# Kernel optimization log

Hardware: AMD Instinct MI355X
Metric: run time of the kernel (lower is better)

## Reference

```python
import jax, jax.numpy as jnp
import numpy as np

DK, DV, NH, KS, STRIDE = 256, 256, 8, 3, 1
PAD = (KS - 1) // 2


def conv1d(x, w, b, stride=1, pad=PAD):
    # x: (B, Cin, W), w: (Cout, Cin, K)
    y = jax.lax.conv_general_dilated(
        x, w, window_strides=(stride,), padding=[(pad, pad)],
        dimension_numbers=("NCH", "OIH", "NCH"))
    return y + b[None, :, None]


def setup_inputs() -> dict:
    key = jax.random.key(0)
    ks = jax.random.split(key, 7)
    B, C, W = 8, 256, 2048
    OUT = 512
    x = jax.random.normal(ks[0], (B, C, W), dtype=jnp.float32)
    w_conv = jax.random.normal(ks[1], (OUT - DV, C, KS), dtype=jnp.float32) * 0.05
    b_conv = jax.random.normal(ks[2], (OUT - DV,), dtype=jnp.float32) * 0.05
    w_qkv = jax.random.normal(ks[3], (2 * DK + DV, C, KS), dtype=jnp.float32) * 0.05
    b_qkv = jax.random.normal(ks[4], (2 * DK + DV,), dtype=jnp.float32) * 0.05
    w_attn = jax.random.normal(ks[5], (DV, DV), dtype=jnp.float32) * 0.05
    b_attn = jax.random.normal(ks[6], (DV,), dtype=jnp.float32) * 0.05
    return {"x": x, "w_conv": w_conv, "b_conv": b_conv,
            "w_qkv": w_qkv, "b_qkv": b_qkv,
            "w_attn": w_attn, "b_attn": b_attn}


def reference(x, w_conv, b_conv, w_qkv, b_qkv, w_attn, b_attn):
    B, _, _ = x.shape
    dkh, dvh = DK // NH, DV // NH

    conv_out = conv1d(x, w_conv, b_conv, stride=STRIDE)   # (B, out-dv, W)
    W_out = conv_out.shape[-1]

    qkv = conv1d(x, w_qkv, b_qkv, stride=STRIDE)          # (B, 2dk+dv, W)
    q, k, v = jnp.split(qkv, [DK, 2 * DK], axis=1)
    q = q.reshape(B, NH, dkh, W_out) * (dkh ** -0.5)      # flat_q
    k = k.reshape(B, NH, dkh, W_out)                      # flat_k
    v = v.reshape(B, NH, dvh, W_out)                      # flat_v

    # logits = flat_q^T @ flat_k : (B, NH, W, W)
    logits = jnp.einsum("bhdq,bhdk->bhqk", q, k)
    weights = jax.nn.softmax(logits, axis=-1)
    # attn = weights @ flat_v^T : (B, NH, W, dvh)
    attn = jnp.einsum("bhqk,bhdk->bhqd", weights, v)
    # NOTE: original torch code RESHAPES (B,NH,W,dvh)->(B,NH,dvh,1,W) (no transpose),
    # then combines heads to (B, NH*dvh, 1, W). Reproduce faithfully:
    attn = attn.reshape(B, DV, W_out)
    # 1x1 conv on attention output
    attn = jnp.einsum("oc,bcw->bow", w_attn, attn) + b_attn[None, :, None]

    return jnp.concatenate([conv_out, attn], axis=1)      # (B, out_channels, W)
```

## Files before the change

kernel.cpp:

```cpp
#include <hip/hip_runtime.h>

typedef _Float16 f16;
typedef _Float16 f16x8 __attribute__((ext_vector_type(8)));
typedef _Float16 f16x4 __attribute__((ext_vector_type(4)));
typedef _Float16 f16x2 __attribute__((ext_vector_type(2)));
typedef __fp16 fp16x2 __attribute__((ext_vector_type(2)));
typedef float f32x4 __attribute__((ext_vector_type(4)));

static __device__ __forceinline__ f32x4 mfma32(f16x8 a, f16x8 b, f32x4 c) {
  return __builtin_amdgcn_mfma_f32_16x16x32_f16(a, b, c, 0, 0, 0);
}
static __device__ __forceinline__ void gload16(const void* g, void* l) {
  __builtin_amdgcn_global_load_lds(
      (const __attribute__((address_space(1))) unsigned int*)g,
      (__attribute__((address_space(3))) unsigned int*)l, 16, 0, 0);
}
static __device__ __forceinline__ f16x2 exp2pk(float a, float b) {
  union { fp16x2 i; f16x2 o; } u;
  u.i = __builtin_amdgcn_cvt_pkrtz(__builtin_amdgcn_exp2f(a), __builtin_amdgcn_exp2f(b));
  return u.o;
}
static __device__ __forceinline__ f16x8 cat4(f16x2 a, f16x2 b, f16x2 c, f16x2 d) {
  union { f16x2 h2[4]; f16x8 h8; } u;
  u.h2[0] = a; u.h2[1] = b; u.h2[2] = c; u.h2[3] = d;
  return u.h8;
}

#define QSCALE_L2 0.25503626336707584f
#define SH_L2  12.98425536800067f

#define OFF_XT   0
#define OFF_WP   8396800
#define OFF_WA   9969664
#define OFF_BIAS 10100736
#define OFF_Q    10104832
#define OFF_K    18493440
#define OFF_V    26882048
#define OFF_AT   35270656

__global__ __launch_bounds__(256) void prep_x_kernel(const float* __restrict__ x,
                                                     f16* __restrict__ xTc) {
  if (blockIdx.x == 256) {
    for (int i = threadIdx.x; i < 4096; i += 256) {
      int b = i >> 9, r = (i >> 8) & 1, ck = (i >> 5) & 7, ci = i & 31;
      xTc[((size_t)(b * 8 + ck) * 2050 + (r ? 2049 : 0)) * 32 + ci] = (f16)0.f;
    }
    return;
  }
  __shared__ f16 tl[64][258];
  const int b  = blockIdx.x >> 5;
  const int w0 = (blockIdx.x & 31) * 64;
  const int tid = threadIdx.x;

  {
    const int wi = (tid & 15) * 4;
    const int cb = tid >> 4;
#pragma unroll 4
    for (int p = 0; p < 16; ++p) {
      const int c = cb + p * 16;
      const float4 v = *(const float4*)(x + ((size_t)(b * 256 + c) * 2048 + w0 + wi));
      tl[wi + 0][c] = (f16)v.x;
      tl[wi + 1][c] = (f16)v.y;
      tl[wi + 2][c] = (f16)v.z;
      tl[wi + 3][c] = (f16)v.w;
    }
  }
  __syncthreads();

  {
    const int w   = tid >> 2;
    const int ci8 = (tid & 3) * 8;
#pragma unroll
    for (int cgk = 0; cgk < 8; ++cgk) {
      f16x8 v = *(const f16x8*)(&tl[w][cgk * 32 + ci8]);
      *(f16x8*)(xTc + ((size_t)(b * 8 + cgk) * 2050 + 1 + w0 + w) * 32 + ci8) = v;
    }
  }
}

__global__ void prep_w_kernel(const float* __restrict__ wc, const float* __restrict__ bc,
                              const float* __restrict__ wq, const float* __restrict__ bq,
                              const float* __restrict__ wa_in,
                              f16* __restrict__ wpc, f16* __restrict__ wa,
                              float* __restrict__ biasp) {
  const int bid = blockIdx.x, tid = threadIdx.x;
  if (bid < 3072) {
    const int n = bid & 1023, t = bid >> 10, c = tid;
    float v;
    if (n < 256) {
      v = wc[(n * 256 + c) * 3 + t];
    } else {
      const int j = n - 256;
      v = wq[((size_t)j * 256 + c) * 3 + t];
      if (j < 256) v *= QSCALE_L2;
    }
    wpc[((size_t)(t * 8 + (c >> 5)) * 1024 + n) * 32 + (c & 31)] = (f16)v;
  } else if (bid < 3328) {
    const int o = bid - 3072;
    wa[o * 256 + tid] = (f16)wa_in[o * 256 + tid];
  } else {
    for (int n = tid; n < 1024; n += 256) {
      float v = (n < 256) ? bc[n] : ((n < 512) ? bq[n - 256] * QSCALE_L2 : bq[n - 256]);
      biasp[n] = v;
    }
  }
}

__global__ __launch_bounds__(512, 1) void conv_kernel(
    const f16* __restrict__ xTc, const f16* __restrict__ wpc,
    const float* __restrict__ biasp, float* __restrict__ out,
    f16* __restrict__ q_ws, f16* __restrict__ k_ws, f16* __restrict__ v_pk) {
  __shared__ __align__(16) char smA[65536];
  __shared__ __align__(16) char smB[65536];

  const int fid = blockIdx.x;
  const int b   = fid & 7;
  const int g   = fid >> 3;
  const int ocb = (g & 3) * 256;
  const int wb  = (g >> 2) * 256;
  const int tid = threadIdx.x;
  const int wid = tid >> 6, l = tid & 63, lr = l & 15, lg = l >> 4;
  const int wm = wid >> 2, wn = wid & 3;

  f32x4 acc[8][4];
#pragma unroll
  for (int i = 0; i < 8; ++i)
#pragma unroll
    for (int j = 0; j < 4; ++j) acc[i][j] = (f32x4){0.f, 0.f, 0.f, 0.f};

  const int swu = (tid >> 2) * 64 + (((tid & 3) ^ ((tid >> 3) & 3)) * 16);
  const char* agb = (const char*)xTc + (size_t)b * 1049600 + (size_t)wb * 64 + swu;
  const char* bgb = (const char*)wpc + (size_t)ocb * 64 + swu;

  const int sx   = ((lr >> 1) & 3) << 4;
  const int foa0 = (wm * 128 + lr) * 64 + ((lg * 16) ^ sx);
  const int fob0 = (wn * 64 + lr) * 64 + ((lg * 16) ^ sx);

  auto stageA = [&](int kt, int kk) {
    const int t = kt >> 2, ck = ((kt & 3) << 1) | kk;
    const char* src = agb + (size_t)ck * 131200 + t * 64;
    char* dst = smA + ((2 * kt + kk) & 3) * 16384 + tid * 16;
    gload16(src, dst);
    gload16(src + 8192, dst + 8192);
  };
  auto stageB = [&](int kt, int kk) {
    const int t = kt >> 2, ck = ((kt & 3) << 1) | kk;
    const char* src = bgb + (size_t)(t * 8 + ck) * 65536;
    char* dst = smB + ((2 * kt + kk) & 3) * 16384 + tid * 16;
    gload16(src, dst);
    gload16(src + 8192, dst + 8192);
  };

  auto phase = [&](int kt, int mh, int kk) {
    const int slot = (2 * kt + kk) & 3;
    const char* ab = smA + slot * 16384;
    const char* bb = smB + slot * 16384;
    f16x8 af[4], bf[4];
#pragma unroll
    for (int mt = 0; mt < 4; ++mt) af[mt] = *(const f16x8*)(ab + foa0 + mh * 4096 + mt * 1024);
#pragma unroll
    for (int nt = 0; nt < 4; ++nt) bf[nt] = *(const f16x8*)(bb + fob0 + nt * 1024);
    __builtin_amdgcn_s_setprio(1);
#pragma unroll
    for (int mt = 0; mt < 4; ++mt)
#pragma unroll
      for (int nt = 0; nt < 4; ++nt)
        acc[mh * 4 + mt][nt] = mfma32(af[mt], bf[nt], acc[mh * 4 + mt][nt]);
    __builtin_amdgcn_s_setprio(0);
  };

#define VMW(n) asm volatile("s_waitcnt vmcnt(" #n ")" ::: "memory")
#define BAR()  __builtin_amdgcn_s_barrier()
#define SCB()  __builtin_amdgcn_sched_barrier(0)

  stageA(0, 0); stageB(0, 0); stageA(0, 1); stageB(0, 1);

#pragma unroll 1
  for (int kt = 0; kt < 11; ++kt) {
    stageA(kt + 1, 0); VMW(6); BAR(); SCB(); phase(kt, 0, 0);
    stageB(kt + 1, 0);         BAR(); SCB(); phase(kt, 1, 0);
    stageA(kt + 1, 1); VMW(6); BAR(); SCB(); phase(kt, 0, 1);
    stageB(kt + 1, 1);         BAR(); SCB(); phase(kt, 1, 1);
  }
  VMW(4); BAR(); SCB(); phase(11, 0, 0);
          BAR(); SCB(); phase(11, 1, 0);
  VMW(0); BAR(); SCB(); phase(11, 0, 1);
          BAR(); SCB(); phase(11, 1, 1);

#undef VMW
#undef BAR
#undef SCB

#pragma unroll
  for (int nt = 0; nt < 4; ++nt) {
    const int oc = ocb + wn * 64 + nt * 16 + lr;
    const float bias = biasp[oc];
#pragma unroll
    for (int am = 0; am < 8; ++am) {
      const int w0 = wb + wm * 128 + am * 16 + lg * 4;
      const float v0 = acc[am][nt][0] + bias;
      const float v1 = acc[am][nt][1] + bias;
      const float v2 = acc[am][nt][2] + bias;
      const float v3 = acc[am][nt][3] + bias;
      if (oc < 256) {
        float4 o4 = {v0, v1, v2, v3};
        *(float4*)(out + (size_t)(b * 512 + oc) * 2048 + w0) = o4;
      } else if (oc < 768) {
        const int d  = oc - 256;
        f16* dst = (d < 256) ? q_ws : k_ws;
        const int dd = d & 31, h = (d >> 5) & 7;
        f16* p = dst + (size_t)((b * 8 + h) * 2048 + w0) * 32 + dd;
        p[0]  = (f16)v0;
        p[32] = (f16)v1;
        p[64] = (f16)v2;
        p[96] = (f16)v3;
      } else {
        const int d = oc - 768;
        const int dd = d & 31, h = d >> 5;
        f16x4 o4 = {(f16)v0, (f16)v1, (f16)v2, (f16)v3};
        *(f16x4*)(v_pk + (size_t)(b * 8 + h) * 65536 +
                  (w0 >> 7) * 4096 + ((w0 >> 5) & 3) * 1024 + dd * 32 +
                  ((w0 >> 2) & 3) * 8 + ((w0 & 16) ? 4 : 0)) = o4;
      }
    }
  }
}

__global__ __launch_bounds__(512, 4) void attn_kernel(
    const f16* __restrict__ q_ws, const f16* __restrict__ k_ws,
    const f16* __restrict__ v_pk, f16* __restrict__ aT) {
  __shared__ __align__(16) f16 Kl[2][4096];
  __shared__ __align__(16) f16 Vl[2][4096];

  const int fid = blockIdx.x;
  const int qb  = fid >> 6;
  const int bh  = ((fid & 7) << 3) | ((fid >> 3) & 7);
  const int tid = threadIdx.x, wid = tid >> 6, l = tid & 63, lr = l & 15, lg = l >> 4;
  const int b = bh >> 3, h = bh & 7;
  const size_t qk_base = (size_t)bh * 2048 * 32;

  const int u = tid & 255;
  const char* gp = (tid < 256)
      ? (const char*)(k_ws + qk_base) + (u >> 2) * 64 + ((u & 3) ^ ((u >> 3) & 3)) * 16
      : (const char*)(v_pk + (size_t)bh * 65536) + u * 16;
  char* lp = ((tid < 256) ? (char*)(&Kl[0][0]) : (char*)(&Vl[0][0])) + u * 16;

  const int qrow0 = qb * 256 + wid * 32;
  f16x8 qf0 = *(const f16x8*)(q_ws + qk_base + (size_t)(qrow0 + lr) * 32 + lg * 8);
  f16x8 qf1 = *(const f16x8*)(q_ws + qk_base + (size_t)(qrow0 + 16 + lr) * 32 + lg * 8);

  f32x4 accO[2][2];
  f32x4 ssum[2];
#pragma unroll
  for (int i = 0; i < 2; ++i) {
    ssum[i] = (f32x4){0.f, 0.f, 0.f, 0.f};
#pragma unroll
    for (int j = 0; j < 2; ++j) accO[i][j] = (f32x4){0.f, 0.f, 0.f, 0.f};
  }
  const f32x4 minit = {-SH_L2, -SH_L2, -SH_L2, -SH_L2};
  const f16x8 ones8 = {(f16)1.f, (f16)1.f, (f16)1.f, (f16)1.f,
                       (f16)1.f, (f16)1.f, (f16)1.f, (f16)1.f};

  const int kfo = lr * 64 + ((lg * 16) ^ (((lr >> 1) & 3) << 4));
  const int vfo = lr * 64 + lg * 16;

  auto stage = [&](int pb) {
    gload16(gp,        lp + pb * 8192);
    gload16(gp + 4096, lp + pb * 8192 + 4096);
    gp += 8192;
  };

  auto compute = [&](int pb) {
    const char* kbuf = (const char*)(&Kl[0][0]) + pb * 8192;
    const char* vbuf = (const char*)(&Vl[0][0]) + pb * 8192;
    f32x4 s0[8], s1[8];
    __builtin_amdgcn_s_setprio(1);
#pragma unroll
    for (int mt = 0; mt < 8; ++mt) {
      f16x8 kf = *(const f16x8*)(kbuf + kfo + mt * 1024);
      s0[mt] = mfma32(kf, qf0, minit);
      s1[mt] = mfma32(kf, qf1, minit);
    }
    __builtin_amdgcn_s_setprio(0);
#pragma unroll
    for (int ksq = 0; ksq < 4; ++ksq) {
      f16x8 pa0 = cat4(exp2pk(s0[2*ksq][0], s0[2*ksq][1]), exp2pk(s0[2*ksq][2], s0[2*ksq][3]),
                       exp2pk(s0[2*ksq+1][0], s0[2*ksq+1][1]), exp2pk(s0[2*ksq+1][2], s0[2*ksq+1][3]));
      f16x8 pa1 = cat4(exp2pk(s1[2*ksq][0], s1[2*ksq][1]), exp2pk(s1[2*ksq][2], s1[2*ksq][3]),
                       exp2pk(s1[2*ksq+1][0], s1[2*ksq+1][1]), exp2pk(s1[2*ksq+1][2], s1[2*ksq+1][3]));
      f16x8 vf0 = *(const f16x8*)(vbuf + vfo + ksq * 2048);
      f16x8 vf1 = *(const f16x8*)(vbuf + vfo + ksq * 2048 + 1024);
      __builtin_amdgcn_s_setprio(1);
      accO[0][0] = mfma32(vf0, pa0, accO[0][0]);
      accO[0][1] = mfma32(vf0, pa1, accO[0][1]);
      accO[1][0] = mfma32(vf1, pa0, accO[1][0]);
      accO[1][1] = mfma32(vf1, pa1, accO[1][1]);
      ssum[0] = mfma32(ones8, pa0, ssum[0]);
      ssum[1] = mfma32(ones8, pa1, ssum[1]);
      __builtin_amdgcn_s_setprio(0);
    }
  };

#define VMW(n) asm volatile("s_waitcnt vmcnt(" #n ")" ::: "memory")
#define BAR()  __builtin_amdgcn_s_barrier()
#define SCB()  __builtin_amdgcn_sched_barrier(0)

  stage(0);
#pragma unroll 1
  for (int t = 0; t < 15; ++t) {
    stage((t + 1) & 1);
    VMW(2); BAR(); SCB();
    compute(t & 1);
    BAR();
  }
  VMW(0); BAR(); SCB();
  compute(1);

#pragma unroll
  for (int nt = 0; nt < 2; ++nt) {
    const float inv = 1.f / ssum[nt][0];
    const int q = qrow0 + nt * 16 + lr;
    const int cc = h * 32 + (q >> 6);
    const int wr = (q & 63) * 32;
#pragma unroll
    for (int dvt = 0; dvt < 2; ++dvt)
#pragma unroll
      for (int r = 0; r < 4; ++r) {
        const int dv = dvt * 16 + lg * 4 + r;
        aT[((size_t)b * 2048 + wr + dv) * 256 + cc] = (f16)(accO[dvt][nt][r] * inv);
      }
  }
#undef VMW
#undef BAR
#undef SCB
}

__global__ __launch_bounds__(256, 4) void proj_kernel(
    const f16* __restrict__ aT, const f16* __restrict__ wa,
    const float* __restrict__ b_attn, float* __restrict__ out) {
  const int fid = blockIdx.x;
  const int b  = fid & 7;
  const int g  = fid >> 3;
  const int ob = (g & 1) * 128;
  const int wb = (g >> 1) * 128;
  const int tid = threadIdx.x;
  const int wid = tid >> 6, l = tid & 63, lr = l & 15, lg = l >> 4;
  const int wm = wid >> 1, wn = wid & 1;

  f32x4 acc[4][4];
#pragma unroll
  for (int i = 0; i < 4; ++i)
#pragma unroll
    for (int j = 0; j < 4; ++j) acc[i][j] = (f32x4){0.f, 0.f, 0.f, 0.f};

  const f16* ab = aT + (size_t)(b * 2048 + wb + wm * 64 + lr) * 256 + lg * 8;
  const f16* wb_p = wa + (size_t)(ob + wn * 64 + lr) * 256 + lg * 8;

  for (int ks = 0; ks < 8; ++ks) {
    const int co = ks * 32;
    f16x8 af[4], bf[4];
#pragma unroll
    for (int mt = 0; mt < 4; ++mt) af[mt] = *(const f16x8*)(ab + (size_t)mt * 16 * 256 + co);
#pragma unroll
    for (int nt = 0; nt < 4; ++nt) bf[nt] = *(const f16x8*)(wb_p + (size_t)nt * 16 * 256 + co);
    __builtin_amdgcn_s_setprio(1);
#pragma unroll
    for (int mt = 0; mt < 4; ++mt)
#pragma unroll
      for (int nt = 0; nt < 4; ++nt) acc[mt][nt] = mfma32(af[mt], bf[nt], acc[mt][nt]);
    __builtin_amdgcn_s_setprio(0);
  }

#pragma unroll
  for (int nt = 0; nt < 4; ++nt) {
    const int o = ob + wn * 64 + nt * 16 + lr;
    const float bias = b_attn[o];
#pragma unroll
    for (int mt = 0; mt < 4; ++mt) {
      const int w0 = wb + wm * 64 + mt * 16 + lg * 4;
      float4 o4 = {acc[mt][nt][0] + bias, acc[mt][nt][1] + bias,
                   acc[mt][nt][2] + bias, acc[mt][nt][3] + bias};
      *(float4*)(out + (size_t)(b * 512 + 256 + o) * 2048 + w0) = o4;
    }
  }
}

extern "C" void kernel_launch(void* const* d_in, const int* in_sizes, int n_in,
                              void* d_out, int out_size, void* d_ws, size_t ws_size,
                              hipStream_t stream) {
  const float* x      = (const float*)d_in[0];
  const float* w_conv = (const float*)d_in[1];
  const float* b_conv = (const float*)d_in[2];
  const float* w_qkv  = (const float*)d_in[3];
  const float* b_qkv  = (const float*)d_in[4];
  const float* w_attn = (const float*)d_in[5];
  const float* b_attn = (const float*)d_in[6];
  float* out = (float*)d_out;

  char* ws = (char*)d_ws;
  f16*   xTc   = (f16*)(ws + OFF_XT);
  f16*   wpc   = (f16*)(ws + OFF_WP);
  f16*   wa    = (f16*)(ws + OFF_WA);
  float* biasp = (float*)(ws + OFF_BIAS);
  f16*   q_ws  = (f16*)(ws + OFF_Q);
  f16*   k_ws  = (f16*)(ws + OFF_K);
  f16*   v_pk  = (f16*)(ws + OFF_V);
  f16*   aT    = (f16*)(ws + OFF_AT);

  prep_x_kernel<<<257, 256, 0, stream>>>(x, xTc);
  prep_w_kernel<<<3329, 256, 0, stream>>>(w_conv, b_conv, w_qkv, b_qkv, w_attn, wpc, wa, biasp);
  conv_kernel<<<256, 512, 0, stream>>>(xTc, wpc, biasp, out, q_ws, k_ws, v_pk);
  attn_kernel<<<512, 512, 0, stream>>>(q_ws, k_ws, v_pk, aT);
  proj_kernel<<<256, 256, 0, stream>>>(aT, wa, b_attn, out);
}
```

Baseline: 115.2 us.

## Split K and V tile staging to interleave loads with QK and PV phases

The attention loop now issues the K and V tile prefetches separately, with all 512 threads loading one 16-byte chunk of each instead of two half-block groups. The next K tile is issued before the QK^T MFMAs and the next V tile after them, with a wait and barrier before each phase in place of a barrier after the combined compute. The goal is finer-grained overlap of global-to-LDS traffic with the two MFMA phases and shorter stalls on each barrier. The trade-off is more waitcnt/barrier points inside the loop and score registers kept live across the phase split, which may add pressure or serialization.

Result: no change. 116.1 us (+0.7%).

```diff
diff --git a/kernel.cpp b/kernel.cpp
--- a/kernel.cpp
+++ b/kernel.cpp
@@ -239,11 +239,11 @@
   const int b = bh >> 3, h = bh & 7;
   const size_t qk_base = (size_t)bh * 2048 * 32;
 
-  const int u = tid & 255;
-  const char* gp = (tid < 256)
-      ? (const char*)(k_ws + qk_base) + (u >> 2) * 64 + ((u & 3) ^ ((u >> 3) & 3)) * 16
-      : (const char*)(v_pk + (size_t)bh * 65536) + u * 16;
-  char* lp = ((tid < 256) ? (char*)(&Kl[0][0]) : (char*)(&Vl[0][0])) + u * 16;
+  const char* kgp = (const char*)(k_ws + qk_base) +
+                    (tid >> 2) * 64 + ((tid & 3) ^ ((tid >> 3) & 3)) * 16;
+  const char* vgp = (const char*)(v_pk + (size_t)bh * 65536) + tid * 16;
+  char* klp = (char*)(&Kl[0][0]) + tid * 16;
+  char* vlp = (char*)(&Vl[0][0]) + tid * 16;
 
   const int qrow0 = qb * 256 + wid * 32;
   f16x8 qf0 = *(const f16x8*)(q_ws + qk_base + (size_t)(qrow0 + lr) * 32 + lg * 8);
@@ -264,16 +264,13 @@
   const int kfo = lr * 64 + ((lg * 16) ^ (((lr >> 1) & 3) << 4));
   const int vfo = lr * 64 + lg * 16;
 
-  auto stage = [&](int pb) {
-    gload16(gp,        lp + pb * 8192);
-    gload16(gp + 4096, lp + pb * 8192 + 4096);
-    gp += 8192;
-  };
-
-  auto compute = [&](int pb) {
+  auto stageK = [&](int pb) { gload16(kgp, klp + pb * 8192); kgp += 8192; };
+  auto stageV = [&](int pb) { gload16(vgp, vlp + pb * 8192); vgp += 8192; };
+
+  f32x4 s0[8], s1[8];
+
+  auto qk = [&](int pb) {
     const char* kbuf = (const char*)(&Kl[0][0]) + pb * 8192;
-    const char* vbuf = (const char*)(&Vl[0][0]) + pb * 8192;
-    f32x4 s0[8], s1[8];
     __builtin_amdgcn_s_setprio(1);
 #pragma unroll
     for (int mt = 0; mt < 8; ++mt) {
@@ -282,6 +279,10 @@
       s1[mt] = mfma32(kf, qf1, minit);
     }
     __builtin_amdgcn_s_setprio(0);
+  };
+
+  auto pv = [&](int pb) {
+    const char* vbuf = (const char*)(&Vl[0][0]) + pb * 8192;
 #pragma unroll
     for (int ksq = 0; ksq < 4; ++ksq) {
       f16x8 pa0 = cat4(exp2pk(s0[2*ksq][0], s0[2*ksq][1]), exp2pk(s0[2*ksq][2], s0[2*ksq][3]),
@@ -305,16 +306,20 @@
 #define BAR()  __builtin_amdgcn_s_barrier()
 #define SCB()  __builtin_amdgcn_sched_barrier(0)
 
-  stage(0);
+  stageK(0); stageV(0);
 #pragma unroll 1
   for (int t = 0; t < 15; ++t) {
-    stage((t + 1) & 1);
+    stageK((t + 1) & 1);
     VMW(2); BAR(); SCB();
-    compute(t & 1);
-    BAR();
-  }
+    qk(t & 1);
+    stageV((t + 1) & 1);
+    VMW(2); BAR(); SCB();
+    pv(t & 1);
+  }
+  VMW(1); BAR(); SCB();
+  qk(1);
   VMW(0); BAR(); SCB();
-  compute(1);
+  pv(1);
 
 #pragma unroll
   for (int nt = 0; nt < 2; ++nt) {
```
